# Kernel optimization log

Hardware: AMD Instinct MI355X
Metric: run time of the kernel (lower is better)

The kernel has to match this reference:

```python
import jax, jax.numpy as jnp
import numpy as np

B, T, N, E = 8, 16, 2048, 32768
F_IN, C, EDGE_DIM = 32, 32, 1


def setup_inputs() -> dict:
    key = jax.random.key(0)
    ks = jax.random.split(key, 12)
    s = 1.0 / np.sqrt(C)
    x = jax.random.normal(ks[0], (B, T, N, F_IN), jnp.float32)
    edge_index = jax.random.randint(ks[1], (2, E), 0, N)
    edge_attr = jax.random.normal(ks[2], (E, EDGE_DIM), jnp.float32)
    Wl = jax.random.normal(ks[3], (F_IN, C), jnp.float32) * s
    bl = jnp.zeros((C,), jnp.float32)
    Wr = jax.random.normal(ks[4], (F_IN, C), jnp.float32) * s
    br = jnp.zeros((C,), jnp.float32)
    We = jax.random.normal(ks[5], (EDGE_DIM, C), jnp.float32) * s
    att = jax.random.normal(ks[6], (C,), jnp.float32) * s
    out_bias = jnp.zeros((C,), jnp.float32)
    w_ih = jax.random.normal(ks[7], (3 * C, C), jnp.float32) * s
    w_hh = jax.random.normal(ks[8], (3 * C, C), jnp.float32) * s
    b_ih = jnp.zeros((3 * C,), jnp.float32)
    b_hh = jnp.zeros((3 * C,), jnp.float32)
    return dict(x=x, edge_index=edge_index, edge_attr=edge_attr, Wl=Wl, bl=bl,
                Wr=Wr, br=br, We=We, att=att, out_bias=out_bias,
                w_ih=w_ih, w_hh=w_hh, b_ih=b_ih, b_hh=b_hh)


def _gatv2(x, edge_index, edge_attr, Wl, bl, Wr, br, We, att, out_bias):
    # x: [B,T,N,F]; GATv2Conv, heads=1, negative_slope=0.2, self loops w/ mean edge attr
    n = x.shape[2]
    src, dst = edge_index[0], edge_index[1]
    deg = jax.ops.segment_sum(jnp.ones((src.shape[0],), x.dtype), dst, num_segments=n)
    mean_attr = jax.ops.segment_sum(edge_attr, dst, num_segments=n) / jnp.maximum(deg, 1.0)[:, None]
    loop = jnp.arange(n)
    src_a = jnp.concatenate([src, loop])
    dst_a = jnp.concatenate([dst, loop])
    attr_a = jnp.concatenate([edge_attr, mean_attr], axis=0)
    xl = x @ Wl + bl  # [B,T,N,C]
    xr = x @ Wr + br
    e_emb = attr_a @ We  # [E2,C]
    xls = jnp.take(xl, src_a, axis=2)  # [B,T,E2,C]
    m = jax.nn.leaky_relu(xls + jnp.take(xr, dst_a, axis=2) + e_emb, 0.2)
    s = jnp.einsum('btec,c->ebt', m, att)  # [E2,B,T]
    smax = jax.ops.segment_max(s, dst_a, num_segments=n)
    es = jnp.exp(s - smax[dst_a])
    denom = jax.ops.segment_sum(es, dst_a, num_segments=n)
    alpha = es / denom[dst_a]  # segment softmax over incoming edges, [E2,B,T]
    msg = xls * alpha.transpose(1, 2, 0)[..., None]  # [B,T,E2,C]
    out = jax.ops.segment_sum(msg.transpose(2, 0, 1, 3), dst_a, num_segments=n)
    return out.transpose(1, 2, 0, 3) + out_bias  # [B,T,N,C]


def _gru(seq, w_ih, w_hh, b_ih, b_hh):
    # seq: [BN, T, C]; torch GRU gate order r,z,n
    c = seq.shape[-1]

    def step(h, xt):
        gi = xt @ w_ih.T + b_ih
        gh = h @ w_hh.T + b_hh
        ir, iz, inn = jnp.split(gi, 3, axis=-1)
        hr, hz, hn = jnp.split(gh, 3, axis=-1)
        r = jax.nn.sigmoid(ir + hr)
        z = jax.nn.sigmoid(iz + hz)
        nc = jnp.tanh(inn + r * hn)
        h = (1.0 - z) * nc + z * h
        return h, h

    h0 = jnp.zeros((seq.shape[0], c), seq.dtype)
    _, ys = jax.lax.scan(step, h0, seq.transpose(1, 0, 2))
    return ys.transpose(1, 0, 2)


def reference(x, edge_index, edge_attr, Wl, bl, Wr, br, We, att, out_bias, w_ih, w_hh, b_ih, b_hh):
    b, t, n, _ = x.shape
    h = _gatv2(x, edge_index, edge_attr, Wl, bl, Wr, br, We, att, out_bias)
    seq = h.transpose(0, 2, 1, 3).reshape(b * n, t, -1)
    y = _gru(seq, w_ih, w_hh, b_ih, b_hh)
    return y.reshape(b, n, t, -1).transpose(0, 2, 1, 3)
```

## Files before the change

kernel.cpp:

```cpp
#include <hip/hip_runtime.h>

#define N_NODES 2048
#define N_EDGES 32768
#define BT      128
#define TT      16
#define CH      32
#define E2      (N_EDGES + N_NODES)

__global__ void deg_attr_kernel(const int* __restrict__ ei,
                                const float* __restrict__ ea,
                                int* __restrict__ deg, float* __restrict__ asum) {
    int e = blockIdx.x * 256 + threadIdx.x;
    if (e < N_EDGES) {
        int dst = ei[N_EDGES + e];
        atomicAdd(&deg[dst], 1);
        atomicAdd(&asum[dst], ea[e]);
    }
}

__global__ void scan_kernel(const int* __restrict__ deg, int* __restrict__ rowp) {
    int lane = threadIdx.x;
    int base = lane * 32;
    int loc[32];
    int s = 0;
    #pragma unroll
    for (int i = 0; i < 32; ++i) { loc[i] = s; s += deg[base + i] + 1; }
    int inc = s;
    #pragma unroll
    for (int d = 1; d < 64; d <<= 1) {
        int v = __shfl_up(inc, d, 64);
        if (lane >= d) inc += v;
    }
    int excl = inc - s;
    #pragma unroll
    for (int i = 0; i < 32; ++i) rowp[base + i] = excl + loc[i];
    if (lane == 63) rowp[N_NODES] = inc;
}

__global__ void scatter_kernel(const int* __restrict__ ei,
                               const float* __restrict__ ea,
                               const int* __restrict__ deg, const float* __restrict__ asum,
                               const int* __restrict__ rowp, int* __restrict__ fill,
                               int* __restrict__ col, float* __restrict__ attr_s) {
    int e = blockIdx.x * 256 + threadIdx.x;
    if (e >= E2) return;
    int src, dst; float a;
    if (e < N_EDGES) {
        src = ei[e]; dst = ei[N_EDGES + e]; a = ea[e];
    } else {
        int n = e - N_EDGES;
        src = n; dst = n;
        a = asum[n] / fmaxf((float)deg[n], 1.0f);
    }
    int pos = atomicAdd(&fill[dst], 1);
    col[rowp[dst] + pos]    = src;
    attr_s[rowp[dst] + pos] = a;
}

__global__ __launch_bounds__(256) void proj_kernel(
        const float* __restrict__ x,
        const float* __restrict__ Wl, const float* __restrict__ bl,
        const float* __restrict__ Wr, const float* __restrict__ br,
        float* __restrict__ xlt, float* __restrict__ xr) {
    __shared__ float xs[128 * 32];
    __shared__ float wl[1024], wr[1024];
    int n = blockIdx.x;
    int tid = threadIdx.x;
    for (int i = tid; i < 1024; i += 256) { wl[i] = Wl[i]; wr[i] = Wr[i]; }
    #pragma unroll
    for (int i = 0; i < 16; ++i) {
        int e = i * 256 + tid;
        int bt = e >> 5, f = e & 31;
        xs[e] = x[((long)bt * N_NODES + n) * 32 + f];
    }
    __syncthreads();
    int c = tid & 31;
    int btl = tid >> 5;
    float blc = bl[c], brc = br[c];
    for (int i = 0; i < 16; ++i) {
        int bt = i * 8 + btl;
        float al = 0.f, ar = 0.f;
        #pragma unroll
        for (int f = 0; f < 32; ++f) {
            float xv = xs[bt * 32 + f];
            al += xv * wl[f * 32 + c];
            ar += xv * wr[f * 32 + c];
        }
        xlt[((long)n * 32 + c) * 128 + bt]   = al + blc;
        xr[((long)bt * N_NODES + n) * 32 + c] = ar + brc;
    }
}

__global__ __launch_bounds__(256) void gat_kernel(
        const float* __restrict__ xlt,
        const float* __restrict__ xr,
        const int* __restrict__ rowp, const int* __restrict__ col,
        const float* __restrict__ attr_s,
        const float* __restrict__ We, const float* __restrict__ att,
        const float* __restrict__ ob,
        float* __restrict__ out) {
    int tid = threadIdx.x;
    int wv = tid >> 6, lane = tid & 63;
    int task = blockIdx.x * 4 + wv;
    int n   = task >> 1;
    int bt  = ((task & 1) << 6) | lane;

    float Wec[32], attc[32];
    #pragma unroll
    for (int c = 0; c < 32; ++c) { Wec[c] = We[c]; attc[c] = att[c]; }

    float xrv[32], accv[32];
    const float* xrp = xr + ((long)bt * N_NODES + n) * CH;
    #pragma unroll
    for (int c = 0; c < 32; ++c) { xrv[c] = xrp[c]; accv[c] = 0.f; }

    int beg = rowp[n];
    int end = rowp[n + 1];
    float den = 0.f;
    const float* xbase = xlt + bt;
    for (int j = beg; j < end; ++j) {
        int   src = col[j];
        float av  = attr_s[j];
        const float* gp = xbase + (long)src * (CH * 128);
        float xlv[32];
        #pragma unroll
        for (int c = 0; c < 32; ++c) xlv[c] = gp[c * 128];
        float p0 = 0.f, p1 = 0.f, p2 = 0.f, p3 = 0.f;
        #pragma unroll
        for (int k = 0; k < 8; ++k) {
            { int c = k;      float m = xlv[c] + fmaf(av, Wec[c], xrv[c]); p0 = fmaf(attc[c], fmaxf(m, 0.2f * m), p0); }
            { int c = k + 8;  float m = xlv[c] + fmaf(av, Wec[c], xrv[c]); p1 = fmaf(attc[c], fmaxf(m, 0.2f * m), p1); }
            { int c = k + 16; float m = xlv[c] + fmaf(av, Wec[c], xrv[c]); p2 = fmaf(attc[c], fmaxf(m, 0.2f * m), p2); }
            { int c = k + 24; float m = xlv[c] + fmaf(av, Wec[c], xrv[c]); p3 = fmaf(attc[c], fmaxf(m, 0.2f * m), p3); }
        }
        float p = fminf((p0 + p1) + (p2 + p3), 80.f);
        float w = __expf(p);
        den += w;
        #pragma unroll
        for (int c = 0; c < 32; ++c) accv[c] = fmaf(w, xlv[c], accv[c]);
    }
    float inv = 1.f / den;
    float* op = out + ((long)bt * N_NODES + n) * CH;
    #pragma unroll
    for (int c = 0; c < 32; ++c) op[c] = fmaf(accv[c], inv, ob[c]);
}

__global__ __launch_bounds__(256, 2) void gru_kernel(
        const float* __restrict__ wih, const float* __restrict__ whh,
        const float* __restrict__ bih, const float* __restrict__ bhh,
        float* hio) {
    int tid  = threadIdx.x;
    int lane = tid & 63;
    int c    = tid & 31;
    int sbase = lane & 32;
    int seq  = blockIdx.x * 8 + (tid >> 5);
    int b = seq >> 11;
    int n = seq & 2047;

    float wi0[32], wi1[32], wi2[32], wh0[32], wh1[32], wh2[32];
    #pragma unroll
    for (int f4 = 0; f4 < 8; ++f4) {
        float4 a;
        a = *(const float4*)&wih[( 0 + c) * 32 + f4 * 4]; wi0[f4*4]=a.x; wi0[f4*4+1]=a.y; wi0[f4*4+2]=a.z; wi0[f4*4+3]=a.w;
        a = *(const float4*)&wih[(32 + c) * 32 + f4 * 4]; wi1[f4*4]=a.x; wi1[f4*4+1]=a.y; wi1[f4*4+2]=a.z; wi1[f4*4+3]=a.w;
        a = *(const float4*)&wih[(64 + c) * 32 + f4 * 4]; wi2[f4*4]=a.x; wi2[f4*4+1]=a.y; wi2[f4*4+2]=a.z; wi2[f4*4+3]=a.w;
        a = *(const float4*)&whh[( 0 + c) * 32 + f4 * 4]; wh0[f4*4]=a.x; wh0[f4*4+1]=a.y; wh0[f4*4+2]=a.z; wh0[f4*4+3]=a.w;
        a = *(const float4*)&whh[(32 + c) * 32 + f4 * 4]; wh1[f4*4]=a.x; wh1[f4*4+1]=a.y; wh1[f4*4+2]=a.z; wh1[f4*4+3]=a.w;
        a = *(const float4*)&whh[(64 + c) * 32 + f4 * 4]; wh2[f4*4]=a.x; wh2[f4*4+1]=a.y; wh2[f4*4+2]=a.z; wh2[f4*4+3]=a.w;
    }
    float bi0 = bih[c], bi1 = bih[32 + c], bi2 = bih[64 + c];
    float bh0 = bhh[c], bh1 = bhh[32 + c], bh2 = bhh[64 + c];

    const long STR = (long)N_NODES * CH;
    long base = ((long)b * TT) * STR + (long)n * CH + c;

    float hc = 0.f;
    float xv = hio[base];
    #pragma unroll 1
    for (int t = 0; t < TT; ++t) {
        float xnext = (t + 1 < TT) ? hio[base + (long)(t + 1) * STR] : 0.f;
        float gx0 = bi0, gx1 = bi1, gx2 = bi2;
        float gh0 = bh0, gh1 = bh1, gh2 = bh2;
        #pragma unroll
        for (int f = 0; f < 32; ++f) {
            float xf = __shfl(xv, sbase | f, 64);
            float hf = __shfl(hc, sbase | f, 64);
            gx0 = fmaf(xf, wi0[f], gx0);
            gx1 = fmaf(xf, wi1[f], gx1);
            gx2 = fmaf(xf, wi2[f], gx2);
            gh0 = fmaf(hf, wh0[f], gh0);
            gh1 = fmaf(hf, wh1[f], gh1);
            gh2 = fmaf(hf, wh2[f], gh2);
        }
        float r  = 1.f / (1.f + __expf(-(gx0 + gh0)));
        float z  = 1.f / (1.f + __expf(-(gx1 + gh1)));
        float a  = gx2 + r * gh2;
        float e2 = __expf(2.f * a);
        float nc = 1.f - 2.f / (e2 + 1.f);
        hc = (1.f - z) * nc + z * hc;
        hio[base + (long)t * STR] = hc;
        xv = xnext;
    }
}

extern "C" void kernel_launch(void* const* d_in, const int* in_sizes, int n_in,
                              void* d_out, int out_size, void* d_ws, size_t ws_size,
                              hipStream_t stream) {
    const float* x    = (const float*)d_in[0];
    const int*   ei   = (const int*)d_in[1];
    const float* ea   = (const float*)d_in[2];
    const float* Wl   = (const float*)d_in[3];
    const float* bl   = (const float*)d_in[4];
    const float* Wr   = (const float*)d_in[5];
    const float* br   = (const float*)d_in[6];
    const float* We   = (const float*)d_in[7];
    const float* att  = (const float*)d_in[8];
    const float* ob   = (const float*)d_in[9];
    const float* wih  = (const float*)d_in[10];
    const float* whh  = (const float*)d_in[11];
    const float* bih  = (const float*)d_in[12];
    const float* bhh  = (const float*)d_in[13];
    float* out = (float*)d_out;

    const long RB = (long)BT * N_NODES * CH;
    int*   deg  = (int*)d_ws;
    float* asum = (float*)(deg + N_NODES);
    int*   fill = (int*)(asum + N_NODES);
    int*   rowp = fill + N_NODES;
    int*   col  = rowp + (N_NODES + 16);
    float* attr_s = (float*)(col + E2);
    float* xlt  = (float*)(attr_s + E2);
    xlt = (float*)(((uintptr_t)xlt + 255) & ~(uintptr_t)255);
    float* xr   = xlt + RB;

    hipMemsetAsync(deg, 0, 3 * N_NODES * sizeof(int), stream);

    deg_attr_kernel<<<N_EDGES / 256, 256, 0, stream>>>(ei, ea, deg, asum);
    scan_kernel<<<1, 64, 0, stream>>>(deg, rowp);
    scatter_kernel<<<(E2 + 255) / 256, 256, 0, stream>>>(ei, ea, deg, asum, rowp, fill, col, attr_s);
    proj_kernel<<<N_NODES, 256, 0, stream>>>(x, Wl, bl, Wr, br, xlt, xr);
    gat_kernel<<<(N_NODES * 2) / 4, 256, 0, stream>>>(xlt, xr, rowp, col, attr_s, We, att, ob, out);
    gru_kernel<<<(BT / TT * N_NODES) / 8, 256, 0, stream>>>(wih, whh, bih, bhh, out);
}
```

Baseline: 267.3 us.

## Split GRU input and hidden matvecs across wavefront halves

The GRU kernel now gives each sequence a full 64-lane wavefront instead of half of one. The lower 32 lanes compute the input-gate matvec and the upper 32 lanes compute the hidden-gate matvec, and the partial sums are combined with a cross-half shuffle. This halves the per-thread weight registers (96 instead of 192 floats) and allows higher occupancy (launch bounds raised to 4), at the cost of twice as many threads, extra shuffles, and duplicated gate math across the halves.

```diff
diff --git a/kernel.cpp b/kernel.cpp
--- a/kernel.cpp
+++ b/kernel.cpp
@@ -145,31 +145,32 @@
     for (int c = 0; c < 32; ++c) op[c] = fmaf(accv[c], inv, ob[c]);
 }
 
-__global__ __launch_bounds__(256, 2) void gru_kernel(
+__global__ __launch_bounds__(256, 4) void gru_kernel(
         const float* __restrict__ wih, const float* __restrict__ whh,
         const float* __restrict__ bih, const float* __restrict__ bhh,
-        float* hio) {
+        float* __restrict__ hio) {
     int tid  = threadIdx.x;
     int lane = tid & 63;
-    int c    = tid & 31;
+    int c    = lane & 31;
+    int half = lane >> 5;
     int sbase = lane & 32;
-    int seq  = blockIdx.x * 8 + (tid >> 5);
+    int seq  = blockIdx.x * 4 + (tid >> 6);
     int b = seq >> 11;
     int n = seq & 2047;
 
-    float wi0[32], wi1[32], wi2[32], wh0[32], wh1[32], wh2[32];
+    const float* W  = half ? whh : wih;
+    const float* Bs = half ? bhh : bih;
+    float w0[32], w1[32], w2[32];
     #pragma unroll
     for (int f4 = 0; f4 < 8; ++f4) {
-        float4 a;
-        a = *(const float4*)&wih[( 0 + c) * 32 + f4 * 4]; wi0[f4*4]=a.x; wi0[f4*4+1]=a.y; wi0[f4*4+2]=a.z; wi0[f4*4+3]=a.w;
-        a = *(const float4*)&wih[(32 + c) * 32 + f4 * 4]; wi1[f4*4]=a.x; wi1[f4*4+1]=a.y; wi1[f4*4+2]=a.z; wi1[f4*4+3]=a.w;
-        a = *(const float4*)&wih[(64 + c) * 32 + f4 * 4]; wi2[f4*4]=a.x; wi2[f4*4+1]=a.y; wi2[f4*4+2]=a.z; wi2[f4*4+3]=a.w;
-        a = *(const float4*)&whh[( 0 + c) * 32 + f4 * 4]; wh0[f4*4]=a.x; wh0[f4*4+1]=a.y; wh0[f4*4+2]=a.z; wh0[f4*4+3]=a.w;
-        a = *(const float4*)&whh[(32 + c) * 32 + f4 * 4]; wh1[f4*4]=a.x; wh1[f4*4+1]=a.y; wh1[f4*4+2]=a.z; wh1[f4*4+3]=a.w;
-        a = *(const float4*)&whh[(64 + c) * 32 + f4 * 4]; wh2[f4*4]=a.x; wh2[f4*4+1]=a.y; wh2[f4*4+2]=a.z; wh2[f4*4+3]=a.w;
-    }
-    float bi0 = bih[c], bi1 = bih[32 + c], bi2 = bih[64 + c];
-    float bh0 = bhh[c], bh1 = bhh[32 + c], bh2 = bhh[64 + c];
+        float4 a0 = *(const float4*)&W[( 0 + c) * 32 + f4 * 4];
+        float4 a1 = *(const float4*)&W[(32 + c) * 32 + f4 * 4];
+        float4 a2 = *(const float4*)&W[(64 + c) * 32 + f4 * 4];
+        w0[f4*4+0]=a0.x; w0[f4*4+1]=a0.y; w0[f4*4+2]=a0.z; w0[f4*4+3]=a0.w;
+        w1[f4*4+0]=a1.x; w1[f4*4+1]=a1.y; w1[f4*4+2]=a1.z; w1[f4*4+3]=a1.w;
+        w2[f4*4+0]=a2.x; w2[f4*4+1]=a2.y; w2[f4*4+2]=a2.z; w2[f4*4+3]=a2.w;
+    }
+    float b0 = Bs[c], b1 = Bs[32 + c], b2 = Bs[64 + c];
 
     const long STR = (long)N_NODES * CH;
     long base = ((long)b * TT) * STR + (long)n * CH + c;
@@ -179,26 +180,27 @@
     #pragma unroll 1
     for (int t = 0; t < TT; ++t) {
         float xnext = (t + 1 < TT) ? hio[base + (long)(t + 1) * STR] : 0.f;
-        float gx0 = bi0, gx1 = bi1, gx2 = bi2;
-        float gh0 = bh0, gh1 = bh1, gh2 = bh2;
+        float src = half ? hc : xv;
+        float g0 = b0, g1 = b1, g2 = b2;
         #pragma unroll
         for (int f = 0; f < 32; ++f) {
-            float xf = __shfl(xv, sbase | f, 64);
-            float hf = __shfl(hc, sbase | f, 64);
-            gx0 = fmaf(xf, wi0[f], gx0);
-            gx1 = fmaf(xf, wi1[f], gx1);
-            gx2 = fmaf(xf, wi2[f], gx2);
-            gh0 = fmaf(hf, wh0[f], gh0);
-            gh1 = fmaf(hf, wh1[f], gh1);
-            gh2 = fmaf(hf, wh2[f], gh2);
+            float v = __shfl(src, sbase | f, 64);
+            g0 = fmaf(v, w0[f], g0);
+            g1 = fmaf(v, w1[f], g1);
+            g2 = fmaf(v, w2[f], g2);
         }
-        float r  = 1.f / (1.f + __expf(-(gx0 + gh0)));
-        float z  = 1.f / (1.f + __expf(-(gx1 + gh1)));
-        float a  = gx2 + r * gh2;
+        float p0 = g0 + __shfl_xor(g0, 32, 64);
+        float p1 = g1 + __shfl_xor(g1, 32, 64);
+        float q2 = __shfl_xor(g2, 32, 64);
+        float gx2 = half ? q2 : g2;
+        float gh2 = half ? g2 : q2;
+        float r  = 1.f / (1.f + __expf(-p0));
+        float z  = 1.f / (1.f + __expf(-p1));
+        float a  = fmaf(r, gh2, gx2);
         float e2 = __expf(2.f * a);
         float nc = 1.f - 2.f / (e2 + 1.f);
         hc = (1.f - z) * nc + z * hc;
-        hio[base + (long)t * STR] = hc;
+        if (half == 0) hio[base + (long)t * STR] = hc;
         xv = xnext;
     }
 }
@@ -240,5 +242,5 @@
     scatter_kernel<<<(E2 + 255) / 256, 256, 0, stream>>>(ei, ea, deg, asum, rowp, fill, col, attr_s);
     proj_kernel<<<N_NODES, 256, 0, stream>>>(x, Wl, bl, Wr, br, xlt, xr);
     gat_kernel<<<(N_NODES * 2) / 4, 256, 0, stream>>>(xlt, xr, rowp, col, attr_s, We, att, ob, out);
-    gru_kernel<<<(BT / TT * N_NODES) / 8, 256, 0, stream>>>(wih, whh, bih, bhh, out);
-}
+    gru_kernel<<<(BT / TT * N_NODES) / 4, 256, 0, stream>>>(wih, whh, bih, bhh, out);
+}
```

Result: slower. 290.0 us (+8.5%).
